# Kernel optimization log

Hardware: AMD Instinct MI355X
Metric: run time of the kernel (lower is better)

Reference implementation:

```python
import jax, jax.numpy as jnp
import numpy as np


def setup_inputs() -> dict:
    key = jax.random.key(0)
    kx, kq, kk, kv = jax.random.split(key, 4)
    B, S, F, D = 4, 4096, 512, 64
    x = jax.random.normal(kx, (B, S, F), dtype=jnp.float32)
    Wq = jax.random.normal(kq, (F, D), dtype=jnp.float32) * 0.05
    Wk = jax.random.normal(kk, (F, D), dtype=jnp.float32) * 0.05
    Wv = jax.random.normal(kv, (F, D), dtype=jnp.float32) * 0.05
    return {"x": x, "Wq": Wq, "Wk": Wk, "Wv": Wv}


def reference(x, Wq, Wk, Wv):
    # x: [B,S,F]; Wq/Wk/Wv: [F,D]
    q = jnp.einsum('bsf,fd->bsd', x, Wq)
    k = jnp.einsum('bsf,fd->bsd', x, Wk)
    v = jnp.einsum('bsf,fd->bsd', x, Wv)
    scale = 1.0 / jnp.sqrt(jnp.asarray(Wq.shape[-1], dtype=x.dtype))
    scores = jnp.einsum('bqd,bkd->bqk', q, k) * scale  # [B,S,S]
    weights = jax.nn.softmax(scores, axis=-1)
    return jnp.einsum('bqk,bkd->bqd', weights, v)
```

## Files before the change

### kernel.cpp

```cpp
#include <hip/hip_runtime.h>

constexpr int Bc = 4, Sc = 4096, Fc = 512, Dc = 64;
constexpr int SPLIT = 8;
constexpr int KT = 64;
constexpr int TILES = (Sc / SPLIT) / KT;

typedef __attribute__((ext_vector_type(8)))  short  short8;
typedef __attribute__((ext_vector_type(4)))  float  float4v;
typedef __attribute__((ext_vector_type(16))) float  float16v;
typedef __attribute__((ext_vector_type(2)))  unsigned int uint2v;

__device__ inline unsigned short f2bf(float f) {
    union { float f; unsigned u; } v; v.f = f;
    unsigned r = v.u + 0x7FFF + ((v.u >> 16) & 1);
    return (unsigned short)(r >> 16);
}
__device__ inline unsigned pk2(float a, float b) {
    union { float f; unsigned u; } x, y; x.f = a; y.f = b;
    unsigned ra = x.u + 0x7FFF + ((x.u >> 16) & 1);
    unsigned rb = y.u + 0x7FFF + ((y.u >> 16) & 1);
    return (ra >> 16) | (rb & 0xFFFF0000u);
}
__device__ inline unsigned cvtpk2(float lo, float hi) {
    unsigned r;
    asm("v_cvt_pk_bf16_f32 %0, %1, %2" : "=v"(r) : "v"(lo), "v"(hi));
    return r;
}
__device__ inline float exp2fast(float x) {
#if defined(__has_builtin) && __has_builtin(__builtin_amdgcn_exp2f)
    return __builtin_amdgcn_exp2f(x);
#else
    return __expf(x * 0.69314718055994531f);
#endif
}

__device__ inline void swap32(unsigned& a, unsigned& b) {
#if defined(__has_builtin) && __has_builtin(__builtin_amdgcn_permlane32_swap)
    uint2v r = __builtin_amdgcn_permlane32_swap(a, b, false, false);
    a = r[0]; b = r[1];
#else
    unsigned ax = (unsigned)__shfl_xor((int)a, 32);
    unsigned bx = (unsigned)__shfl_xor((int)b, 32);
    int upper = (threadIdx.x & 32) != 0;
    unsigned na = upper ? bx : a;
    unsigned nb = upper ? b  : ax;
    a = na; b = nb;
#endif
}

__global__ __launch_bounds__(256) void prep_kernel(
    const float* __restrict__ Wq, const float* __restrict__ Wk,
    const float* __restrict__ Wv, unsigned short* __restrict__ Wf)
{
    int wi = blockIdx.x * 256 + threadIdx.x;
    int lane = wi & 63;
    int kc = (wi >> 6) & 15;
    int nt = wi >> 10;
    int lm = lane & 15, quad = lane >> 4;
    int n = nt * 16 + lm;
    const float* W = (n < 64) ? Wq : (n < 128) ? Wk : Wv;
    int nc = n & 63;
    float scale = (n < 64) ? 0.18033688011112042f : 1.0f;
    int kbase = kc * 32 + quad * 8;
    union { uint4 v; unsigned short s[8]; } tmp;
    #pragma unroll
    for (int j = 0; j < 8; ++j)
        tmp.s[j] = f2bf(W[(size_t)(kbase + j) * Dc + nc] * scale);
    *(uint4*)&Wf[(size_t)wi * 8] = tmp.v;
}

__global__ __launch_bounds__(256) void qkv_kernel(
    const float* __restrict__ x, const unsigned short* __restrict__ Wf,
    unsigned short* __restrict__ Qb, unsigned short* __restrict__ Kb,
    unsigned short* __restrict__ Vtb)
{
    __shared__ __align__(16) unsigned short Xs[2][16][72];
    __shared__ __align__(16) unsigned short Ot[16][200];
    const int t = threadIdx.x;
    const int lane = t & 63, w = t >> 6;
    const int lm = lane & 15, quad = lane >> 4;
    const int row0 = blockIdx.x * 16;
    const int sr = t >> 4, sc4 = (t & 15) * 4;

    float4 xv;
    auto load_x = [&](int k0) {
        xv = *(const float4*)&x[(size_t)(row0 + sr) * Fc + k0 + sc4];
    };
    load_x(0);

    float4v acc[3];
    #pragma unroll
    for (int n = 0; n < 3; ++n) acc[n] = float4v{0.f, 0.f, 0.f, 0.f};

    int buf = 0;
    #pragma unroll
    for (int k0 = 0; k0 < Fc; k0 += 64, buf ^= 1) {
        uint2 pk;
        pk.x = pk2(xv.x, xv.y); pk.y = pk2(xv.z, xv.w);
        *(uint2*)&Xs[buf][sr][sc4] = pk;
        __syncthreads();
        if (k0 + 64 < Fc) load_x(k0 + 64);

        short8 af[2];
        #pragma unroll
        for (int h = 0; h < 2; ++h)
            af[h] = *(const short8*)&Xs[buf][lm][h * 32 + quad * 8];

        #pragma unroll
        for (int n = 0; n < 3; ++n) {
            const int nt = 3 * w + n;
            #pragma unroll
            for (int h = 0; h < 2; ++h) {
                const int kchunk = (k0 >> 5) + h;
                short8 bf_ = *(const short8*)&Wf[(size_t)((nt * 16 + kchunk) * 64 + lane) * 8];
                acc[n] = __builtin_amdgcn_mfma_f32_16x16x32_bf16(af[h], bf_, acc[n], 0, 0, 0);
            }
        }
    }

    __syncthreads();
    #pragma unroll
    for (int n = 0; n < 3; ++n)
        #pragma unroll
        for (int r = 0; r < 4; ++r)
            Ot[quad * 4 + r][(3 * w + n) * 16 + lm] = f2bf(acc[n][r]);
    __syncthreads();

    {
        const int r2 = t >> 4, c2 = (t & 15) * 4;
        *(uint2*)&Qb[(size_t)(row0 + r2) * Dc + c2] = *(const uint2*)&Ot[r2][c2];
        *(uint2*)&Kb[(size_t)(row0 + r2) * Dc + c2] = *(const uint2*)&Ot[r2][64 + c2];
    }
    {
        const int d = t >> 2, s4 = (t & 3) * 4;
        union { uint2 v; unsigned short s[4]; } tmp;
        #pragma unroll
        for (int j = 0; j < 4; ++j) tmp.s[j] = Ot[s4 + j][128 + d];
        const int bb = row0 >> 12, s0r = row0 & (Sc - 1);
        *(uint2*)&Vtb[((size_t)bb * Dc + d) * Sc + s0r + s4] = tmp.v;
    }
}

__global__ __launch_bounds__(256) void attn_kernel(
    const unsigned short* __restrict__ Qb, const unsigned short* __restrict__ Kb,
    const unsigned short* __restrict__ Vtb,
    float* __restrict__ Op, float* __restrict__ lp)
{
    __shared__ __align__(16) char smem[36864];

    const int t = threadIdx.x;
    const int lane = t & 63, w = t >> 6;
    const int l31 = lane & 31, lh = lane >> 5;
    const int b = blockIdx.y, z = blockIdx.z;
    const int q0 = blockIdx.x * 128 + w * 32;
    const size_t qkbase = (size_t)b * Sc * Dc;
    const size_t vbase  = (size_t)b * Dc * Sc;
    const int k0base = z * (Sc / SPLIT);

    short8 qf[4];
    #pragma unroll
    for (int c = 0; c < 4; ++c)
        qf[c] = *(const short8*)&Qb[qkbase + (size_t)(q0 + l31) * Dc + c * 16 + lh * 8];

    float16v O0, O1;
    #pragma unroll
    for (int r = 0; r < 16; ++r) { O0[r] = 0.f; O1[r] = 0.f; }
    float lA = 0.f, lB = 0.f;

    const int rowInW = lane >> 3;
    const int srcChunk = (lane & 7) ^ rowInW;
    auto stage = [&](int p, int k0) {
        char* base = smem + p * 16384;
        #pragma unroll
        for (int j = 0; j < 2; ++j) {
            const int row = w * 16 + j * 8 + rowInW;
            const unsigned short* gk = Kb + qkbase + (size_t)(k0 + row) * Dc + srcChunk * 8;
            const unsigned short* gv = Vtb + vbase + (size_t)row * Sc + k0 + srcChunk * 8;
            __builtin_amdgcn_global_load_lds(
                (const __attribute__((address_space(1))) void*)gk,
                (__attribute__((address_space(3))) void*)(base + (w * 16 + j * 8) * 128),
                16, 0, 0);
            __builtin_amdgcn_global_load_lds(
                (const __attribute__((address_space(1))) void*)gv,
                (__attribute__((address_space(3))) void*)(base + 8192 + (w * 16 + j * 8) * 128),
                16, 0, 0);
        }
    };

    const int rx = l31 & 7;
    auto rd = [&](const char* buf, int row, int cc) -> short8 {
        return *(const short8*)(buf + row * 128 + ((cc ^ rx) * 16));
    };

    auto mk_pb = [&](const float16v& s, int g) -> short8 {
        unsigned X0 = cvtpk2(s[8 * g + 0], s[8 * g + 1]);
        unsigned X1 = cvtpk2(s[8 * g + 2], s[8 * g + 3]);
        unsigned Y0 = cvtpk2(s[8 * g + 4], s[8 * g + 5]);
        unsigned Y1 = cvtpk2(s[8 * g + 6], s[8 * g + 7]);
        swap32(X0, Y0);
        swap32(X1, Y1);
        union { unsigned u[4]; short8 s8; } r;
        r.u[0] = X0; r.u[1] = X1; r.u[2] = Y0; r.u[3] = Y1;
        return r.s8;
    };

    stage(0, k0base);
    stage(1, k0base + KT);

    int p = 0;
    for (int kt = 0; kt < TILES; ++kt, p ^= 1) {
        if (kt + 1 < TILES) { asm volatile("s_waitcnt vmcnt(4)" ::: "memory"); }
        else                { asm volatile("s_waitcnt vmcnt(0)" ::: "memory"); }
        __builtin_amdgcn_sched_barrier(0);
        __builtin_amdgcn_s_barrier();
        __builtin_amdgcn_sched_barrier(0);

        const char* kb = smem + p * 16384;
        const char* vb = kb + 8192;

        float16v s0, s1;
        #pragma unroll
        for (int r = 0; r < 16; ++r) { s0[r] = 0.f; s1[r] = 0.f; }
        __builtin_amdgcn_s_setprio(1);
        #pragma unroll
        for (int c = 0; c < 4; ++c) {
            short8 a0 = rd(kb, l31,      2 * c + lh);
            short8 a1 = rd(kb, 32 + l31, 2 * c + lh);
            s0 = __builtin_amdgcn_mfma_f32_32x32x16_bf16(a0, qf[c], s0, 0, 0, 0);
            s1 = __builtin_amdgcn_mfma_f32_32x32x16_bf16(a1, qf[c], s1, 0, 0, 0);
        }
        __builtin_amdgcn_s_setprio(0);

        #pragma unroll
        for (int r = 0; r < 16; ++r) {
            float p0 = exp2fast(s0[r]); s0[r] = p0; lA += p0;
            float p1 = exp2fast(s1[r]); s1[r] = p1; lB += p1;
        }

        short8 pb0 = mk_pb(s0, 0);
        short8 pb1 = mk_pb(s0, 1);
        short8 pb2 = mk_pb(s1, 0);
        short8 pb3 = mk_pb(s1, 1);

        __builtin_amdgcn_s_setprio(1);
        #pragma unroll
        for (int c = 0; c < 4; ++c) {
            short8 pb  = (c == 0) ? pb0 : (c == 1) ? pb1 : (c == 2) ? pb2 : pb3;
            short8 va0 = rd(vb, l31,      2 * c + lh);
            short8 va1 = rd(vb, 32 + l31, 2 * c + lh);
            O0 = __builtin_amdgcn_mfma_f32_32x32x16_bf16(va0, pb, O0, 0, 0, 0);
            O1 = __builtin_amdgcn_mfma_f32_32x32x16_bf16(va1, pb, O1, 0, 0, 0);
        }
        __builtin_amdgcn_s_setprio(0);

        asm volatile("s_waitcnt lgkmcnt(0)" ::: "memory");
        __builtin_amdgcn_sched_barrier(0);
        __builtin_amdgcn_s_barrier();
        if (kt + 2 < TILES) stage(p, k0base + (kt + 2) * KT);
    }

    float l_i = lA + lB;
    l_i += __shfl_xor(l_i, 32);

    __syncthreads();
    float* Of = (float*)(smem + w * 8704);
    #pragma unroll
    for (int r = 0; r < 16; ++r) {
        int d0 = (r & 3) + 8 * (r >> 2) + 4 * lh;
        Of[l31 * 68 + d0]      = O0[r];
        Of[l31 * 68 + 32 + d0] = O1[r];
    }
    const size_t obase = ((size_t)(z * Bc + b) * Sc + q0) * Dc;
    const int qr = lane >> 4, c4 = (lane & 15) * 4;
    #pragma unroll
    for (int i = 0; i < 8; ++i) {
        int q = i * 4 + qr;
        *(float4*)&Op[obase + (size_t)q * Dc + c4] = *(const float4*)&Of[q * 68 + c4];
    }
    if (lane < 32)
        lp[(z * Bc + b) * Sc + q0 + l31] = l_i;
}

__global__ __launch_bounds__(256) void combine_kernel(
    const float* __restrict__ Op, const float* __restrict__ lp,
    float* __restrict__ out)
{
    const int BS = Bc * Sc;
    int tid = blockIdx.x * 256 + threadIdx.x;
    int bq = tid >> 4, dc = (tid & 15) * 4;
    float L = 0.f;
    #pragma unroll
    for (int zz = 0; zz < SPLIT; ++zz) L += lp[zz * BS + bq];
    float inv = 1.f / L;
    size_t o = (size_t)bq * Dc + dc;
    size_t stride = (size_t)BS * Dc;
    float4 r = {0.f, 0.f, 0.f, 0.f};
    #pragma unroll
    for (int zz = 0; zz < SPLIT; ++zz) {
        float4 pz = *(const float4*)&Op[o + zz * stride];
        r.x += pz.x; r.y += pz.y; r.z += pz.z; r.w += pz.w;
    }
    r.x *= inv; r.y *= inv; r.z *= inv; r.w *= inv;
    *(float4*)&out[o] = r;
}

extern "C" void kernel_launch(void* const* d_in, const int* in_sizes, int n_in,
                              void* d_out, int out_size, void* d_ws, size_t ws_size,
                              hipStream_t stream) {
    const float* x  = (const float*)d_in[0];
    const float* Wq = (const float*)d_in[1];
    const float* Wk = (const float*)d_in[2];
    const float* Wv = (const float*)d_in[3];
    float* out = (float*)d_out;

    char* p = (char*)d_ws;
    unsigned short* Wf  = (unsigned short*)p;  p += (size_t)192 * Fc * 2;
    unsigned short* Qb  = (unsigned short*)p;  p += (size_t)Bc * Sc * Dc * 2;
    unsigned short* Kb  = (unsigned short*)p;  p += (size_t)Bc * Sc * Dc * 2;
    unsigned short* Vtb = (unsigned short*)p;  p += (size_t)Bc * Sc * Dc * 2;
    float* lp = (float*)p;                     p += (size_t)SPLIT * Bc * Sc * 4;
    float* Op = (float*)p;

    prep_kernel<<<48, 256, 0, stream>>>(Wq, Wk, Wv, Wf);
    qkv_kernel<<<Bc * Sc / 16, 256, 0, stream>>>(x, Wf, Qb, Kb, Vtb);
    attn_kernel<<<dim3(Sc / 128, Bc, SPLIT), 256, 0, stream>>>(Qb, Kb, Vtb, Op, lp);
    combine_kernel<<<(Bc * Sc * 16) / 256, 256, 0, stream>>>(Op, lp, out);
}
```

Baseline: 121.0 us.

## Fuse split-K combine into attention kernel via last-block atomic semaphore

Removes the separate combine kernel. Each attention block bumps an atomic counter per (query tile, batch) once its partial output is written, and the last of the SPLIT blocks to arrive reduces the partial outputs and row sums into the final output. Counters are zeroed in the prep kernel. This saves one kernel launch and its tail, at the cost of fences, an atomic per block, and serial reduction work in the last-arriving blocks.

```diff
diff --git a/kernel.cpp b/kernel.cpp
--- a/kernel.cpp
+++ b/kernel.cpp
@@ -50,9 +50,11 @@
 
 __global__ __launch_bounds__(256) void prep_kernel(
     const float* __restrict__ Wq, const float* __restrict__ Wk,
-    const float* __restrict__ Wv, unsigned short* __restrict__ Wf)
+    const float* __restrict__ Wv, unsigned short* __restrict__ Wf,
+    unsigned* __restrict__ sem)
 {
     int wi = blockIdx.x * 256 + threadIdx.x;
+    if (wi < (Sc / 128) * Bc) sem[wi] = 0u;
     int lane = wi & 63;
     int kc = (wi >> 6) & 15;
     int nt = wi >> 10;
@@ -144,9 +146,11 @@
 __global__ __launch_bounds__(256) void attn_kernel(
     const unsigned short* __restrict__ Qb, const unsigned short* __restrict__ Kb,
     const unsigned short* __restrict__ Vtb,
-    float* __restrict__ Op, float* __restrict__ lp)
+    float* __restrict__ Op, float* __restrict__ lp,
+    unsigned* __restrict__ sem, float* __restrict__ out)
 {
     __shared__ __align__(16) char smem[36864];
+    __shared__ int lastFlag;
 
     const int t = threadIdx.x;
     const int lane = t & 63, w = t >> 6;
@@ -279,29 +283,39 @@
     }
     if (lane < 32)
         lp[(z * Bc + b) * Sc + q0 + l31] = l_i;
-}
-
-__global__ __launch_bounds__(256) void combine_kernel(
-    const float* __restrict__ Op, const float* __restrict__ lp,
-    float* __restrict__ out)
-{
-    const int BS = Bc * Sc;
-    int tid = blockIdx.x * 256 + threadIdx.x;
-    int bq = tid >> 4, dc = (tid & 15) * 4;
-    float L = 0.f;
-    #pragma unroll
-    for (int zz = 0; zz < SPLIT; ++zz) L += lp[zz * BS + bq];
-    float inv = 1.f / L;
-    size_t o = (size_t)bq * Dc + dc;
-    size_t stride = (size_t)BS * Dc;
-    float4 r = {0.f, 0.f, 0.f, 0.f};
-    #pragma unroll
-    for (int zz = 0; zz < SPLIT; ++zz) {
-        float4 pz = *(const float4*)&Op[o + zz * stride];
-        r.x += pz.x; r.y += pz.y; r.z += pz.z; r.w += pz.w;
-    }
-    r.x *= inv; r.y *= inv; r.z *= inv; r.w *= inv;
-    *(float4*)&out[o] = r;
+
+    __syncthreads();
+    if (t == 0) {
+        __threadfence();
+        unsigned old = atomicAdd(&sem[blockIdx.x * Bc + b], 1u);
+        lastFlag = (old == SPLIT - 1);
+        __threadfence();
+    }
+    __syncthreads();
+    if (lastFlag) {
+        const int BS = Bc * Sc;
+        const int q0b = blockIdx.x * 128;
+        const size_t stride = (size_t)BS * Dc;
+        #pragma unroll
+        for (int i = 0; i < 8; ++i) {
+            int unit = i * 256 + t;
+            int q = unit >> 4, dc = (unit & 15) * 4;
+            int bq = b * Sc + q0b + q;
+            float L = 0.f;
+            #pragma unroll
+            for (int zz = 0; zz < SPLIT; ++zz) L += lp[zz * BS + bq];
+            float inv = 1.f / L;
+            size_t o = (size_t)bq * Dc + dc;
+            float4 r = {0.f, 0.f, 0.f, 0.f};
+            #pragma unroll
+            for (int zz = 0; zz < SPLIT; ++zz) {
+                float4 pz = *(const float4*)&Op[o + zz * stride];
+                r.x += pz.x; r.y += pz.y; r.z += pz.z; r.w += pz.w;
+            }
+            r.x *= inv; r.y *= inv; r.z *= inv; r.w *= inv;
+            *(float4*)&out[o] = r;
+        }
+    }
 }
 
 extern "C" void kernel_launch(void* const* d_in, const int* in_sizes, int n_in,
@@ -319,10 +333,10 @@
     unsigned short* Kb  = (unsigned short*)p;  p += (size_t)Bc * Sc * Dc * 2;
     unsigned short* Vtb = (unsigned short*)p;  p += (size_t)Bc * Sc * Dc * 2;
     float* lp = (float*)p;                     p += (size_t)SPLIT * Bc * Sc * 4;
+    unsigned* sem = (unsigned*)p;              p += 4096;
     float* Op = (float*)p;
 
-    prep_kernel<<<48, 256, 0, stream>>>(Wq, Wk, Wv, Wf);
+    prep_kernel<<<48, 256, 0, stream>>>(Wq, Wk, Wv, Wf, sem);
     qkv_kernel<<<Bc * Sc / 16, 256, 0, stream>>>(x, Wf, Qb, Kb, Vtb);
-    attn_kernel<<<dim3(Sc / 128, Bc, SPLIT), 256, 0, stream>>>(Qb, Kb, Vtb, Op, lp);
-    combine_kernel<<<(Bc * Sc * 16) / 256, 256, 0, stream>>>(Op, lp, out);
-}
+    attn_kernel<<<dim3(Sc / 128, Bc, SPLIT), 256, 0, stream>>>(Qb, Kb, Vtb, Op, lp, sem, out);
+}
```

Measured after the change: 181.7 us. 1.5x slower.
